# Performance work log

Hardware: AMD Instinct MI355X
Metric: run time of the kernel (lower is better)

Reference implementation:

```python
import jax, jax.numpy as jnp
from jax import lax
import numpy as np

B, CIN, COUT, N, H, W = 16, 64, 64, 8, 128, 128


def setup_inputs() -> dict:
    key = jax.random.key(0)
    ks = jax.random.split(key, 6)
    s = 0.05
    return {
        "x": jax.random.normal(ks[0], (B, CIN, H, W), dtype=jnp.float32),
        "condition": jax.random.normal(ks[1], (B, CIN), dtype=jnp.float32),
        "filt_w": jax.random.normal(ks[2], (N, COUT, CIN, 3, 3), dtype=jnp.float32) * s,
        "filt_b": jax.random.normal(ks[3], (N, COUT), dtype=jnp.float32) * s,
        "sel_w": jax.random.normal(ks[4], (N, CIN), dtype=jnp.float32) * s,
        "sel_b": jax.random.normal(ks[5], (N,), dtype=jnp.float32) * s,
    }


def reference(x, condition, filt_w, filt_b, sel_w, sel_b):
    b = x.shape[0]
    # condition selector: Linear(in_channels -> num_conditions) + softmax
    logits = condition.reshape(b, -1) @ sel_w.T + sel_b          # [B, N]
    weights = jax.nn.softmax(logits, axis=-1)                    # [B, N]

    n, cout, cin, kh, kw = filt_w.shape
    # Run all N branch convs in ONE conv by stacking filters on the output-channel axis.
    kern = filt_w.reshape(n * cout, cin, kh, kw)
    y = lax.conv_general_dilated(
        x, kern, window_strides=(1, 1), padding="SAME",
        dimension_numbers=("NCHW", "OIHW", "NCHW"))              # [B, N*COUT, H, W]
    h, w = y.shape[-2], y.shape[-1]
    y = y.reshape(b, n, cout, h, w) + filt_b.reshape(1, n, cout, 1, 1)
    # softmax-gated sum over the N branches
    out = jnp.einsum("bn,bnohw->bohw", weights, y)
    return out
```

## Files before the change

### kernel.cpp

```cpp
#include <hip/hip_runtime.h>
#include <stdint.h>

#define BATCH 16
#define CIN   64
#define COUT  64
#define NBR   8
#define HH    128
#define WW    128

typedef __attribute__((ext_vector_type(8)))  short short8;
typedef __attribute__((ext_vector_type(16))) float f32x16;

__device__ __forceinline__ unsigned int f2bf_hi(float f) {
    union { float f; uint32_t u; } v; v.f = f;
    return (v.u + 0x8000u) >> 16;
}
__device__ __forceinline__ unsigned short f2bf(float f) {
    union { float f; uint32_t u; } v; v.f = f;
    uint32_t u = v.u;
    return (unsigned short)((u + 0x7FFFu + ((u >> 16) & 1u)) >> 16);
}
__device__ __forceinline__ short8 gld_frag(const unsigned short* p) {
    union { uint4 u; short8 s; } t;
    t.u = *(const uint4*)p;
    return t.s;
}
__device__ __forceinline__ short8 lds_frag(const unsigned short* p) {
    union { uint2 u[2]; short8 s; } t;
    t.u[0] = *(const uint2*)p;
    t.u[1] = *(const uint2*)(p + 4);
    return t.s;
}

__global__ __launch_bounds__(256)
void k_prep(const float* __restrict__ cond,
            const float* __restrict__ sel_w,
            const float* __restrict__ sel_b,
            const float* __restrict__ filt_w,
            const float* __restrict__ filt_b,
            unsigned short* __restrict__ wfilt,
            float* __restrict__ cbias) {
    __shared__ float lg[BATCH][NBR];
    const int tid = threadIdx.x;
    if (tid < BATCH * NBR) {
        int b2 = tid >> 3, n = tid & 7;
        float acc = sel_b[n];
        #pragma unroll
        for (int c = 0; c < CIN; ++c)
            acc += cond[b2 * CIN + c] * sel_w[n * CIN + c];
        lg[b2][n] = acc;
    }
    __syncthreads();

    const int idx = blockIdx.x * 256 + tid;
    const int b  = idx >> 12;
    const int oc = idx & 4095;
    const int o  = oc >> 6, c = oc & 63;

    float w8[NBR];
    {
        float m = -1e30f;
        #pragma unroll
        for (int n = 0; n < NBR; ++n) m = fmaxf(m, lg[b][n]);
        float s = 0.f;
        #pragma unroll
        for (int n = 0; n < NBR; ++n) { w8[n] = __expf(lg[b][n] - m); s += w8[n]; }
        float inv = 1.f / s;
        #pragma unroll
        for (int n = 0; n < NBR; ++n) w8[n] *= inv;
    }

    float acc[9];
    #pragma unroll
    for (int t = 0; t < 9; ++t) acc[t] = 0.f;
    #pragma unroll
    for (int n = 0; n < NBR; ++n) {
        const float* p = filt_w + ((long)(n * COUT + o) * CIN + c) * 9;
        #pragma unroll
        for (int t = 0; t < 9; ++t) acc[t] += w8[n] * p[t];
    }
    #pragma unroll
    for (int t = 0; t < 9; ++t)
        wfilt[((long)(b * 9 + t) * 4096) + oc] = f2bf(acc[t]);

    if (oc < COUT) {
        float ab = 0.f;
        #pragma unroll
        for (int n = 0; n < NBR; ++n) ab += w8[n] * filt_b[n * COUT + oc];
        cbias[b * COUT + oc] = ab;
    }
}

#define RT 8
#define WT 32
#define SLABW 34
#define SLABR 10
#define PSTR  68

__global__ __launch_bounds__(256, 3)
void k_conv3(const float* __restrict__ x,
             const unsigned short* __restrict__ wfilt,
             const float* __restrict__ cbias,
             float* __restrict__ out) {
    __shared__ unsigned short lx[SLABR * SLABW * PSTR];

    const int b  = blockIdx.z;
    const int h0 = blockIdx.y * RT;
    const int w0 = blockIdx.x * WT;
    const int tid = threadIdx.x;

    for (int task = tid; task < SLABR * 32 * 10; task += 256) {
        const int j  = task % 10;
        const int r  = task / 10;
        const int cp = r & 31;
        const int s  = r >> 5;
        const int c  = cp * 2;
        const int hin   = h0 + s - 1;
        const int wbase = w0 - 4 + j * 4;
        float4 v0, v1;
        v0.x = v0.y = v0.z = v0.w = 0.f;
        v1 = v0;
        if (hin >= 0 && hin < HH && wbase >= 0 && wbase < WW) {
            const float* px = x + (((long)(b * CIN + c) * HH + hin) * WW + wbase);
            v0 = *(const float4*)px;
            v1 = *(const float4*)(px + (long)HH * WW);
        }
        unsigned int d[4];
        d[0] = f2bf_hi(v0.x) | (f2bf_hi(v1.x) << 16);
        d[1] = f2bf_hi(v0.y) | (f2bf_hi(v1.y) << 16);
        d[2] = f2bf_hi(v0.z) | (f2bf_hi(v1.z) << 16);
        d[3] = f2bf_hi(v0.w) | (f2bf_hi(v1.w) << 16);
        #pragma unroll
        for (int i = 0; i < 4; ++i) {
            const int p = j * 4 - 3 + i;
            if (p >= 0 && p < SLABW)
                *(unsigned int*)&lx[(s * SLABW + p) * PSTR + c] = d[i];
        }
    }

    const int lane = tid & 63;
    const int wave = tid >> 6;
    const int l31  = lane & 31;
    const int lh   = lane >> 5;
    const int r0   = wave * 2;

    f32x16 acc00, acc01, acc10, acc11;
    #pragma unroll
    for (int i = 0; i < 16; ++i) {
        const int m = (i & 3) + 8 * (i >> 2) + 4 * lh;
        const float b0 = cbias[b * COUT + m];
        const float b1 = cbias[b * COUT + 32 + m];
        acc00[i] = b0; acc01[i] = b0;
        acc10[i] = b1; acc11[i] = b1;
    }

    __syncthreads();

    const unsigned short* wf = wfilt + (long)b * 9 * COUT * CIN;

    #pragma unroll
    for (int tap = 0; tap < 9; ++tap) {
        const int kh = tap / 3, kw = tap % 3;
        const unsigned short* wft = wf + (long)tap * COUT * CIN;
        #pragma unroll
        for (int cc = 0; cc < 4; ++cc) {
            const int kofs = cc * 16 + lh * 8;
            short8 a0 = gld_frag(wft + l31 * CIN + kofs);
            short8 a1 = gld_frag(wft + (32 + l31) * CIN + kofs);
            short8 b0 = lds_frag(&lx[((r0     + kh) * SLABW + l31 + kw) * PSTR + kofs]);
            short8 b1 = lds_frag(&lx[((r0 + 1 + kh) * SLABW + l31 + kw) * PSTR + kofs]);
            acc00 = __builtin_amdgcn_mfma_f32_32x32x16_bf16(a0, b0, acc00, 0, 0, 0);
            acc01 = __builtin_amdgcn_mfma_f32_32x32x16_bf16(a0, b1, acc01, 0, 0, 0);
            acc10 = __builtin_amdgcn_mfma_f32_32x32x16_bf16(a1, b0, acc10, 0, 0, 0);
            acc11 = __builtin_amdgcn_mfma_f32_32x32x16_bf16(a1, b1, acc11, 0, 0, 0);
        }
    }

    #pragma unroll
    for (int cb = 0; cb < 2; ++cb) {
        #pragma unroll
        for (int pb = 0; pb < 2; ++pb) {
            const f32x16 v = cb == 0 ? (pb == 0 ? acc00 : acc01)
                                     : (pb == 0 ? acc10 : acc11);
            const int hrow = h0 + r0 + pb;
            float* op = out + (((long)(b * COUT + cb * 32) * HH + hrow) * WW + w0 + l31);
            #pragma unroll
            for (int i = 0; i < 16; ++i) {
                const int m = (i & 3) + 8 * (i >> 2) + 4 * lh;
                op[(long)m * HH * WW] = v[i];
            }
        }
    }
}

extern "C" void kernel_launch(void* const* d_in, const int* in_sizes, int n_in,
                              void* d_out, int out_size, void* d_ws, size_t ws_size,
                              hipStream_t stream) {
    const float* x      = (const float*)d_in[0];
    const float* cond   = (const float*)d_in[1];
    const float* filt_w = (const float*)d_in[2];
    const float* filt_b = (const float*)d_in[3];
    const float* sel_w  = (const float*)d_in[4];
    const float* sel_b  = (const float*)d_in[5];
    float* out = (float*)d_out;

    float*          cbias = (float*)d_ws;
    unsigned short* wfilt = (unsigned short*)((char*)d_ws + 4096);

    k_prep<<<256, 256, 0, stream>>>(cond, sel_w, sel_b, filt_w, filt_b, wfilt, cbias);

    dim3 grid(WW / WT, HH / RT, BATCH);
    k_conv3<<<grid, 256, 0, stream>>>(x, wfilt, cbias, out);
}
```

Before: 192.2 us.

## Restage filter-mix prep through LDS and prefetch next-tap weights in conv

The prep kernel now runs one block per (batch, output channel). Each block stages that channel's filter slices for all eight branches into shared memory with float4 loads and computes the logits with a wave reduction, replacing the strided per-thread global reads. The conv kernel keeps the current tap's A fragments in registers and issues global loads for the next tap before the MFMAs, so the weight fetch latency overlaps with compute. The extra registers this needs are paid for by lowering the launch-bounds occupancy hint from 3 to 2 blocks per CU, which may reduce latency hiding.

```diff
diff --git a/kernel.cpp b/kernel.cpp
--- a/kernel.cpp
+++ b/kernel.cpp
@@ -40,54 +40,61 @@
             const float* __restrict__ filt_b,
             unsigned short* __restrict__ wfilt,
             float* __restrict__ cbias) {
-    __shared__ float lg[BATCH][NBR];
+    __shared__ float4 lw4[NBR * 144];
+    __shared__ float lg[NBR];
+    float* lw = (float*)lw4;
+
+    const int blk = blockIdx.x;
+    const int b = blk >> 6, o = blk & 63;
     const int tid = threadIdx.x;
-    if (tid < BATCH * NBR) {
-        int b2 = tid >> 3, n = tid & 7;
-        float acc = sel_b[n];
-        #pragma unroll
-        for (int c = 0; c < CIN; ++c)
-            acc += cond[b2 * CIN + c] * sel_w[n * CIN + c];
-        lg[b2][n] = acc;
+
+    const float4* src4 = (const float4*)filt_w;
+    #pragma unroll
+    for (int i = tid; i < NBR * 144; i += 256)
+        lw4[i] = src4[((i / 144) * COUT + o) * 144 + (i % 144)];
+
+    {
+        const int lane = tid & 63, w = tid >> 6;
+        const float c0 = cond[b * CIN + lane];
+        #pragma unroll
+        for (int k = 0; k < 2; ++k) {
+            const int n = w + k * 4;
+            float p = c0 * sel_w[n * CIN + lane];
+            #pragma unroll
+            for (int off = 32; off > 0; off >>= 1)
+                p += __shfl_down(p, off, 64);
+            if (lane == 0) lg[n] = p + sel_b[n];
+        }
     }
     __syncthreads();
-
-    const int idx = blockIdx.x * 256 + tid;
-    const int b  = idx >> 12;
-    const int oc = idx & 4095;
-    const int o  = oc >> 6, c = oc & 63;
 
     float w8[NBR];
     {
         float m = -1e30f;
         #pragma unroll
-        for (int n = 0; n < NBR; ++n) m = fmaxf(m, lg[b][n]);
+        for (int n = 0; n < NBR; ++n) m = fmaxf(m, lg[n]);
         float s = 0.f;
         #pragma unroll
-        for (int n = 0; n < NBR; ++n) { w8[n] = __expf(lg[b][n] - m); s += w8[n]; }
-        float inv = 1.f / s;
+        for (int n = 0; n < NBR; ++n) { w8[n] = __expf(lg[n] - m); s += w8[n]; }
+        const float inv = 1.f / s;
         #pragma unroll
         for (int n = 0; n < NBR; ++n) w8[n] *= inv;
     }
 
-    float acc[9];
-    #pragma unroll
-    for (int t = 0; t < 9; ++t) acc[t] = 0.f;
-    #pragma unroll
-    for (int n = 0; n < NBR; ++n) {
-        const float* p = filt_w + ((long)(n * COUT + o) * CIN + c) * 9;
-        #pragma unroll
-        for (int t = 0; t < 9; ++t) acc[t] += w8[n] * p[t];
-    }
-    #pragma unroll
-    for (int t = 0; t < 9; ++t)
-        wfilt[((long)(b * 9 + t) * 4096) + oc] = f2bf(acc[t]);
-
-    if (oc < COUT) {
+    #pragma unroll
+    for (int idx = tid; idx < 576; idx += 256) {
+        const int t = idx >> 6, c = idx & 63;
+        float acc = 0.f;
+        #pragma unroll
+        for (int n = 0; n < NBR; ++n)
+            acc += w8[n] * lw[n * 576 + c * 9 + t];
+        wfilt[(((long)(b * 9 + t) * COUT + o) << 6) + c] = f2bf(acc);
+    }
+    if (tid == 0) {
         float ab = 0.f;
         #pragma unroll
-        for (int n = 0; n < NBR; ++n) ab += w8[n] * filt_b[n * COUT + oc];
-        cbias[b * COUT + oc] = ab;
+        for (int n = 0; n < NBR; ++n) ab += w8[n] * filt_b[n * COUT + o];
+        cbias[b * COUT + o] = ab;
     }
 }
 
@@ -97,8 +104,8 @@
 #define SLABR 10
 #define PSTR  68
 
-__global__ __launch_bounds__(256, 3)
-void k_conv3(const float* __restrict__ x,
+__global__ __launch_bounds__(256, 2)
+void k_conv4(const float* __restrict__ x,
              const unsigned short* __restrict__ wfilt,
              const float* __restrict__ cbias,
              float* __restrict__ out) {
@@ -144,6 +151,15 @@
     const int lh   = lane >> 5;
     const int r0   = wave * 2;
 
+    const unsigned short* wf = wfilt + (long)b * 9 * COUT * CIN;
+
+    short8 A0[4], A1[4];
+    #pragma unroll
+    for (int cc = 0; cc < 4; ++cc) {
+        A0[cc] = gld_frag(wf + l31 * CIN + cc * 16 + lh * 8);
+        A1[cc] = gld_frag(wf + (32 + l31) * CIN + cc * 16 + lh * 8);
+    }
+
     f32x16 acc00, acc01, acc10, acc11;
     #pragma unroll
     for (int i = 0; i < 16; ++i) {
@@ -156,24 +172,30 @@
 
     __syncthreads();
 
-    const unsigned short* wf = wfilt + (long)b * 9 * COUT * CIN;
-
     #pragma unroll
     for (int tap = 0; tap < 9; ++tap) {
+        short8 nA0[4], nA1[4];
+        if (tap < 8) {
+            const unsigned short* wn = wf + (long)(tap + 1) * COUT * CIN;
+            #pragma unroll
+            for (int cc = 0; cc < 4; ++cc) {
+                nA0[cc] = gld_frag(wn + l31 * CIN + cc * 16 + lh * 8);
+                nA1[cc] = gld_frag(wn + (32 + l31) * CIN + cc * 16 + lh * 8);
+            }
+        }
         const int kh = tap / 3, kw = tap % 3;
-        const unsigned short* wft = wf + (long)tap * COUT * CIN;
         #pragma unroll
         for (int cc = 0; cc < 4; ++cc) {
             const int kofs = cc * 16 + lh * 8;
-            short8 a0 = gld_frag(wft + l31 * CIN + kofs);
-            short8 a1 = gld_frag(wft + (32 + l31) * CIN + kofs);
             short8 b0 = lds_frag(&lx[((r0     + kh) * SLABW + l31 + kw) * PSTR + kofs]);
             short8 b1 = lds_frag(&lx[((r0 + 1 + kh) * SLABW + l31 + kw) * PSTR + kofs]);
-            acc00 = __builtin_amdgcn_mfma_f32_32x32x16_bf16(a0, b0, acc00, 0, 0, 0);
-            acc01 = __builtin_amdgcn_mfma_f32_32x32x16_bf16(a0, b1, acc01, 0, 0, 0);
-            acc10 = __builtin_amdgcn_mfma_f32_32x32x16_bf16(a1, b0, acc10, 0, 0, 0);
-            acc11 = __builtin_amdgcn_mfma_f32_32x32x16_bf16(a1, b1, acc11, 0, 0, 0);
-        }
+            acc00 = __builtin_amdgcn_mfma_f32_32x32x16_bf16(A0[cc], b0, acc00, 0, 0, 0);
+            acc01 = __builtin_amdgcn_mfma_f32_32x32x16_bf16(A0[cc], b1, acc01, 0, 0, 0);
+            acc10 = __builtin_amdgcn_mfma_f32_32x32x16_bf16(A1[cc], b0, acc10, 0, 0, 0);
+            acc11 = __builtin_amdgcn_mfma_f32_32x32x16_bf16(A1[cc], b1, acc11, 0, 0, 0);
+        }
+        #pragma unroll
+        for (int cc = 0; cc < 4; ++cc) { A0[cc] = nA0[cc]; A1[cc] = nA1[cc]; }
     }
 
     #pragma unroll
@@ -207,8 +229,8 @@
     float*          cbias = (float*)d_ws;
     unsigned short* wfilt = (unsigned short*)((char*)d_ws + 4096);
 
-    k_prep<<<256, 256, 0, stream>>>(cond, sel_w, sel_b, filt_w, filt_b, wfilt, cbias);
+    k_prep<<<BATCH * COUT, 256, 0, stream>>>(cond, sel_w, sel_b, filt_w, filt_b, wfilt, cbias);
 
     dim3 grid(WW / WT, HH / RT, BATCH);
-    k_conv3<<<grid, 256, 0, stream>>>(x, wfilt, cbias, out);
-}
+    k_conv4<<<grid, 256, 0, stream>>>(x, wfilt, cbias, out);
+}
```

Result: faster. 176.9 us (-8.0%).
